# Kernel optimization log

Measured on AMD Instinct MI355X. Metric: run time of the kernel, lower is better.

The kernel has to match this reference:

```python
import jax, jax.numpy as jnp
import numpy as np

B, T, E = 2, 2048, 1024   # batch, block_size, emb_d
H, D = 16, 64             # heads, head_size


def setup_inputs() -> dict:
    key = jax.random.key(0)
    ks = jax.random.split(key, 7)
    s = 1.0 / np.sqrt(E)
    inputs = jax.random.normal(ks[0], (B, T, E), dtype=jnp.float32)
    k_w = jax.random.uniform(ks[1], (H, E, D), jnp.float32, -s, s)
    k_b = jax.random.uniform(ks[2], (H, D), jnp.float32, -s, s)
    q_w = jax.random.uniform(ks[3], (H, E, D), jnp.float32, -s, s)
    q_b = jax.random.uniform(ks[4], (H, D), jnp.float32, -s, s)
    v_w = jax.random.uniform(ks[5], (H, E, D), jnp.float32, -s, s)
    v_b = jax.random.uniform(ks[6], (H, D), jnp.float32, -s, s)
    return {"inputs": inputs, "k_w": k_w, "k_b": k_b,
            "q_w": q_w, "q_b": q_b, "v_w": v_w, "v_b": v_b}


def reference(inputs, k_w, k_b, q_w, q_b, v_w, v_b):
    # Per-head linear projections, vectorized over heads: (B,T,E)x(H,E,D)->(B,H,T,D)
    k = jnp.einsum('bte,hed->bhtd', inputs, k_w) + k_b[None, :, None, :]
    q = jnp.einsum('bte,hed->bhtd', inputs, q_w) + q_b[None, :, None, :]
    v = jnp.einsum('bte,hed->bhtd', inputs, v_w) + v_b[None, :, None, :]

    scale = D ** (-0.5)
    # scores: (B,H,Tq,Tk)
    w = jnp.einsum('bhtd,bhsd->bhts', q, k) * scale
    tril = jnp.tril(jnp.ones((T, T), dtype=bool))
    w = jnp.where(tril[None, None, :, :], w, -jnp.inf)
    # NOTE: original torch code does softmax(weights, dim=1) on a (B,T,T)
    # tensor, i.e. over the QUERY axis. Faithfully reproduce: axis=-2 here.
    w = jax.nn.softmax(w, axis=-2)
    out = jnp.einsum('bhts,bhsd->bhtd', w, v)           # (B,H,T,D)
    # concat heads along last dim, head-major order matching torch.cat
    return out.transpose(0, 2, 1, 3).reshape(B, T, H * D)
```

## Files before the change

### kernel.cpp

```cpp
#include <hip/hip_runtime.h>
#include <hip/hip_bf16.h>
#include <math.h>

#define B_ 2
#define T_ 2048
#define E_ 1024
#define H_ 16
#define D_ 64
#define NT_ 32
#define QSCALE 0.180336880f

typedef __attribute__((ext_vector_type(8))) short bf16x8;
typedef __attribute__((ext_vector_type(4))) float f32x4;

#if __has_builtin(__builtin_amdgcn_exp2f)
#define EXP2(x) __builtin_amdgcn_exp2f(x)
#else
#define EXP2(x) exp2f(x)
#endif

__device__ __forceinline__ unsigned short f2bf(float x) {
  union { float f; unsigned u; } v; v.f = x;
  unsigned r = v.u + 0x7FFFu + ((v.u >> 16) & 1u);
  return (unsigned short)(r >> 16);
}
__device__ __forceinline__ unsigned pk2bf(float a, float b) {
  __hip_bfloat162 h = __float22bfloat162_rn(make_float2(a, b));
  union { __hip_bfloat162 h; unsigned u; } c; c.h = h; return c.u;
}

__device__ __forceinline__ void dma8(const unsigned short* g, int gstride,
                                     unsigned short* l, int lane)
{
  const int r = lane >> 3, bg = (lane & 7) ^ (r & 7);
  __builtin_amdgcn_global_load_lds(
      (const __attribute__((address_space(1))) void*)(g + (size_t)r * gstride + bg * 8),
      (__attribute__((address_space(3))) void*)l, 16, 0, 0);
}
__device__ __forceinline__ bf16x8 frag(const unsigned short* tile, int row, int g) {
  return *(const bf16x8*)(tile + row * 64 + (((g ^ row) & 7) << 3));
}

__global__ __launch_bounds__(256) void inpack_kernel(const float* __restrict__ in,
                                                     unsigned short* __restrict__ o) {
  const size_t i = ((size_t)blockIdx.x * 256 + threadIdx.x) * 8;
  float4 f0 = *(const float4*)(in + i);
  float4 f1 = *(const float4*)(in + i + 4);
  unsigned u[4] = { pk2bf(f0.x, f0.y), pk2bf(f0.z, f0.w),
                    pk2bf(f1.x, f1.y), pk2bf(f1.z, f1.w) };
  *(bf16x8*)(o + i) = *(const bf16x8*)u;
}

__global__ __launch_bounds__(256) void wpack_kernel(
    const float* __restrict__ qw, const float* __restrict__ kw, const float* __restrict__ vw,
    unsigned short* __restrict__ qwt, unsigned short* __restrict__ kwt,
    unsigned short* __restrict__ vwt)
{
  __shared__ float s[64][65];
  const int tid = threadIdx.x;
  const int e0 = blockIdx.x * 64, h = blockIdx.y, z = blockIdx.z;
  const float* w = (z == 0) ? qw : (z == 1) ? kw : vw;
  unsigned short* o = (z == 0) ? qwt : (z == 1) ? kwt : vwt;
  {
    const int r = tid >> 2;
    #pragma unroll
    for (int p = 0; p < 4; ++p) {
      const int c = (tid & 3) * 4 + p * 16;
      float4 f = *(const float4*)(w + ((size_t)(h * E_ + e0 + r)) * D_ + c);
      s[r][c] = f.x; s[r][c+1] = f.y; s[r][c+2] = f.z; s[r][c+3] = f.w;
    }
  }
  __syncthreads();
  {
    const int d = tid >> 2, ec = (tid & 3) * 16;
    unsigned short tmp[16];
    #pragma unroll
    for (int j = 0; j < 16; ++j) tmp[j] = f2bf(s[ec + j][d]);
    unsigned short* dst = o + ((size_t)(h * D_ + d)) * E_ + e0 + ec;
    *(bf16x8*)(dst)     = *(const bf16x8*)&tmp[0];
    *(bf16x8*)(dst + 8) = *(const bf16x8*)&tmp[8];
  }
}

__global__ __launch_bounds__(256) void proj_kernel(
    const unsigned short* __restrict__ in16,
    const unsigned short* __restrict__ qwt, const unsigned short* __restrict__ kwt,
    const unsigned short* __restrict__ vwt,
    const float* __restrict__ qb, const float* __restrict__ kb, const float* __restrict__ vb,
    unsigned short* __restrict__ qo, unsigned short* __restrict__ ko,
    unsigned short* __restrict__ vt)
{
  __shared__ __align__(16) unsigned short in_s[2][128 * 64];
  __shared__ __align__(16) unsigned short w_s[2][3][64 * 64];
  const int tid = threadIdx.x;
  const int lane = tid & 63, wv = tid >> 6;
  const int l15 = lane & 15, quad = lane >> 4;
  const int t0 = blockIdx.x * 128, h = blockIdx.y, b = blockIdx.z;
  const int bh = b * H_ + h;
  const unsigned short* wts[3] = { qwt, kwt, vwt };

  f32x4 acc[3][2][4];
  #pragma unroll
  for (int x = 0; x < 3; ++x)
    #pragma unroll
    for (int s = 0; s < 2; ++s)
      #pragma unroll
      for (int nb = 0; nb < 4; ++nb) acc[x][s][nb] = (f32x4){0.f, 0.f, 0.f, 0.f};

#define PROJ_STAGE(e0_, bi_)                                                      \
  {                                                                               \
    const unsigned short* gin = in16 + ((size_t)(b * T_ + t0)) * E_ + (e0_);      \
    _Pragma("unroll")                                                             \
    for (int p = 0; p < 4; ++p) {                                                 \
      const int br = wv * 32 + p * 8;                                             \
      dma8(gin + (size_t)br * E_, E_, &in_s[bi_][br * 64], lane);                 \
    }                                                                             \
    _Pragma("unroll")                                                             \
    for (int j = 0; j < 6; ++j) {                                                 \
      const int idx = wv * 6 + j;                                                 \
      const int x = idx >> 3, br = (idx & 7) * 8;                                 \
      dma8(wts[x] + ((size_t)(h * D_ + br)) * E_ + (e0_), E_,                     \
           &w_s[bi_][x][br * 64], lane);                                          \
    }                                                                             \
  }

  PROJ_STAGE(0, 0);
  __syncthreads();
  for (int e = 0; e < 16; ++e) {
    const int bi = e & 1;
    if (e < 15) PROJ_STAGE((e + 1) * 64, bi ^ 1);
    const unsigned short* is = in_s[bi];
    #pragma unroll
    for (int kk = 0; kk < 2; ++kk) {
      const int g0 = kk * 4 + quad;
      bf16x8 a0 = frag(is, wv * 32 + l15, g0);
      bf16x8 a1 = frag(is, wv * 32 + 16 + l15, g0);
      #pragma unroll
      for (int x = 0; x < 3; ++x) {
        const unsigned short* ws = w_s[bi][x];
        #pragma unroll
        for (int nb = 0; nb < 4; ++nb) {
          bf16x8 bfr = frag(ws, nb * 16 + l15, g0);
          if (x < 2) {
            acc[x][0][nb] = __builtin_amdgcn_mfma_f32_16x16x32_bf16(bfr, a0, acc[x][0][nb], 0, 0, 0);
            acc[x][1][nb] = __builtin_amdgcn_mfma_f32_16x16x32_bf16(bfr, a1, acc[x][1][nb], 0, 0, 0);
          } else {
            acc[x][0][nb] = __builtin_amdgcn_mfma_f32_16x16x32_bf16(a0, bfr, acc[x][0][nb], 0, 0, 0);
            acc[x][1][nb] = __builtin_amdgcn_mfma_f32_16x16x32_bf16(a1, bfr, acc[x][1][nb], 0, 0, 0);
          }
        }
      }
    }
    __syncthreads();
  }
#undef PROJ_STAGE

  const size_t obase = (size_t)bh * T_;
  #pragma unroll
  for (int x = 0; x < 2; ++x) {
    const float scl = (x == 0) ? QSCALE : 1.0f;
    const float* bias = (x == 0) ? qb : kb;
    unsigned short* outp = (x == 0) ? qo : ko;
    #pragma unroll
    for (int nb = 0; nb < 4; ++nb) {
      float bias4[4];
      *(float4*)bias4 = *(const float4*)&bias[h * D_ + nb * 16 + quad * 4];
      #pragma unroll
      for (int s = 0; s < 2; ++s) {
        const int t = t0 + wv * 32 + s * 16 + l15;
        unsigned short pk[4];
        #pragma unroll
        for (int r = 0; r < 4; ++r) pk[r] = f2bf((acc[x][s][nb][r] + bias4[r]) * scl);
        *(ushort4*)(outp + (obase + t) * D_ + nb * 16 + quad * 4) = *(const ushort4*)pk;
      }
    }
  }
  #pragma unroll
  for (int nb = 0; nb < 4; ++nb) {
    const int d = nb * 16 + l15;
    const float bvv = vb[h * D_ + d];
    #pragma unroll
    for (int s = 0; s < 2; ++s) {
      const int t = t0 + wv * 32 + s * 16 + quad * 4;
      unsigned short pk[4];
      #pragma unroll
      for (int r = 0; r < 4; ++r) pk[r] = f2bf(acc[2][s][nb][r] + bvv);
      *(ushort4*)(vt + ((size_t)(bh * D_ + d)) * T_ + t) = *(const ushort4*)pk;
    }
  }
}

__global__ __launch_bounds__(256, 6) void stats_kernel(
    const unsigned short* __restrict__ q, const unsigned short* __restrict__ k,
    float* __restrict__ lg)
{
  __shared__ __align__(16) unsigned short q_s[2][64 * 64];
  __shared__ float red[4][64];
  const int tid = threadIdx.x;
  const int lane = tid & 63, wv = tid >> 6;
  const int l15 = lane & 15, quad = lane >> 4;
  const int h = blockIdx.x, b = blockIdx.y, sa = blockIdx.z;
  const int bh = b * H_ + h;
  const int s0 = sa * 64;
  const unsigned short* qbase = q + (size_t)bh * T_ * 64;

  bf16x8 kf[4][2];
  #pragma unroll
  for (int nb = 0; nb < 4; ++nb)
    #pragma unroll
    for (int kk = 0; kk < 2; ++kk)
      kf[nb][kk] = *(const bf16x8*)(k + ((size_t)(bh * T_ + s0 + nb * 16 + l15)) * 64
                                      + kk * 32 + quad * 8);

  #pragma unroll
  for (int pp = 0; pp < 2; ++pp) {
    const int br = wv * 16 + pp * 8;
    dma8(qbase + (size_t)(sa * 64 + br) * 64, 64, &q_s[0][br * 64], lane);
  }
  __syncthreads();

  float lsum[4] = {0.f, 0.f, 0.f, 0.f};

  for (int tt = sa, i = 0; tt < NT_; ++tt, ++i) {
    const int bi = i & 1;
    if (tt + 1 < NT_) {
      #pragma unroll
      for (int pp = 0; pp < 2; ++pp) {
        const int br = wv * 16 + pp * 8;
        dma8(qbase + (size_t)((tt + 1) * 64 + br) * 64, 64, &q_s[bi ^ 1][br * 64], lane);
      }
    }
    bf16x8 a0 = frag(q_s[bi], wv * 16 + l15, quad);
    bf16x8 a1 = frag(q_s[bi], wv * 16 + l15, 4 + quad);
    f32x4 sacc[4];
    #pragma unroll
    for (int nb = 0; nb < 4; ++nb) sacc[nb] = (f32x4){0.f, 0.f, 0.f, 0.f};
    #pragma unroll
    for (int nb = 0; nb < 4; ++nb) {
      sacc[nb] = __builtin_amdgcn_mfma_f32_16x16x32_bf16(a0, kf[nb][0], sacc[nb], 0, 0, 0);
      sacc[nb] = __builtin_amdgcn_mfma_f32_16x16x32_bf16(a1, kf[nb][1], sacc[nb], 0, 0, 0);
    }
    if (tt == sa) {
      const int tbase = tt * 64 + wv * 16 + quad * 4;
      #pragma unroll
      for (int nb = 0; nb < 4; ++nb) {
        const int s = s0 + nb * 16 + l15;
        #pragma unroll
        for (int r = 0; r < 4; ++r)
          lsum[nb] += (tbase + r >= s) ? EXP2(sacc[nb][r]) : 0.f;
      }
    } else {
      #pragma unroll
      for (int nb = 0; nb < 4; ++nb)
        #pragma unroll
        for (int r = 0; r < 4; ++r) lsum[nb] += EXP2(sacc[nb][r]);
    }
    __syncthreads();
  }
  #pragma unroll
  for (int nb = 0; nb < 4; ++nb) {
    lsum[nb] += __shfl_xor(lsum[nb], 16);
    lsum[nb] += __shfl_xor(lsum[nb], 32);
  }
  if (lane < 16) {
    #pragma unroll
    for (int nb = 0; nb < 4; ++nb) red[wv][nb * 16 + lane] = lsum[nb];
  }
  __syncthreads();
  if (tid < 64) {
    const float L = red[0][tid] + red[1][tid] + red[2][tid] + red[3][tid];
    lg[(size_t)bh * T_ + s0 + tid] = -__log2f(L);
  }
}

__global__ __launch_bounds__(256, 6) void out_kernel(
    const unsigned short* __restrict__ q, const unsigned short* __restrict__ k,
    const unsigned short* __restrict__ vt, const float* __restrict__ lg,
    float* __restrict__ out)
{
  __shared__ __align__(16) unsigned short k_s[64 * 64];
  __shared__ __align__(16) unsigned short vt_s[64 * 64];
  __shared__ __align__(16) unsigned short u_s[4][16][72];
  __shared__ float lg_sh[64];
  const int tid = threadIdx.x;
  const int lane = tid & 63, wv = tid >> 6;
  const int l15 = lane & 15, quad = lane >> 4;
  const int h = blockIdx.x, b = blockIdx.y, jt = 31 - blockIdx.z;
  const int bh = b * H_ + h;
  const int t0 = jt * 64;
  const unsigned short* kbase = k + (size_t)bh * T_ * 64;
  const unsigned short* vbase = vt + (size_t)bh * D_ * T_;
  const float* lgbase = lg + (size_t)bh * T_;

  const unsigned short* qrow = q + (size_t)(bh * T_ + t0 + wv * 16 + l15) * 64;
  bf16x8 qf0 = *(const bf16x8*)(qrow + quad * 8);
  bf16x8 qf1 = *(const bf16x8*)(qrow + 32 + quad * 8);

  f32x4 oacc[4];
  #pragma unroll
  for (int nb = 0; nb < 4; ++nb) oacc[nb] = (f32x4){0.f, 0.f, 0.f, 0.f};

  unsigned short* urow = &u_s[wv][l15][0];
  const int tcol = t0 + wv * 16 + l15;

  for (int st = 0; st <= jt; ++st) {
    const int s0 = st * 64;
    __syncthreads();
    #pragma unroll
    for (int pp = 0; pp < 2; ++pp) {
      const int br = wv * 16 + pp * 8;
      dma8(kbase + (size_t)(s0 + br) * 64, 64, &k_s[br * 64], lane);
      dma8(vbase + (size_t)br * T_ + s0, T_, &vt_s[br * 64], lane);
    }
    if (tid < 64) lg_sh[tid] = lgbase[s0 + tid];
    __syncthreads();
    f32x4 sacc[4];
    #pragma unroll
    for (int mb = 0; mb < 4; ++mb) {
      float lg4[4];
      *(float4*)lg4 = *(const float4*)&lg_sh[mb * 16 + quad * 4];
      sacc[mb] = (f32x4){lg4[0], lg4[1], lg4[2], lg4[3]};
    }
    #pragma unroll
    for (int mb = 0; mb < 4; ++mb) {
      bf16x8 ka0 = frag(k_s, mb * 16 + l15, quad);
      bf16x8 ka1 = frag(k_s, mb * 16 + l15, 4 + quad);
      sacc[mb] = __builtin_amdgcn_mfma_f32_16x16x32_bf16(ka0, qf0, sacc[mb], 0, 0, 0);
      sacc[mb] = __builtin_amdgcn_mfma_f32_16x16x32_bf16(ka1, qf1, sacc[mb], 0, 0, 0);
    }
    if (st == jt) {
      #pragma unroll
      for (int mb = 0; mb < 4; ++mb) {
        const int sbase = s0 + mb * 16 + quad * 4;
        float uu[4] = { EXP2(sacc[mb][0]), EXP2(sacc[mb][1]),
                        EXP2(sacc[mb][2]), EXP2(sacc[mb][3]) };
        #pragma unroll
        for (int r = 0; r < 4; ++r) if (tcol < sbase + r) uu[r] = 0.f;
        *(uint2*)(urow + mb * 16 + quad * 4) =
            make_uint2(pk2bf(uu[0], uu[1]), pk2bf(uu[2], uu[3]));
      }
    } else {
      #pragma unroll
      for (int mb = 0; mb < 4; ++mb) {
        float uu[4] = { EXP2(sacc[mb][0]), EXP2(sacc[mb][1]),
                        EXP2(sacc[mb][2]), EXP2(sacc[mb][3]) };
        *(uint2*)(urow + mb * 16 + quad * 4) =
            make_uint2(pk2bf(uu[0], uu[1]), pk2bf(uu[2], uu[3]));
      }
    }
    #pragma unroll
    for (int kk = 0; kk < 2; ++kk) {
      bf16x8 ua = *(const bf16x8*)(urow + kk * 32 + quad * 8);
      #pragma unroll
      for (int nb = 0; nb < 4; ++nb)
        oacc[nb] = __builtin_amdgcn_mfma_f32_16x16x32_bf16(
            frag(vt_s, nb * 16 + l15, kk * 4 + quad), ua, oacc[nb], 0, 0, 0);
    }
  }
  float* orow = out + ((size_t)(b * T_ + t0 + wv * 16 + l15)) * (H_ * D_) + h * D_;
  #pragma unroll
  for (int nb = 0; nb < 4; ++nb) {
    float o4[4] = { oacc[nb][0], oacc[nb][1], oacc[nb][2], oacc[nb][3] };
    *(float4*)(orow + nb * 16 + quad * 4) = *(const float4*)o4;
  }
}

extern "C" void kernel_launch(void* const* d_in, const int* in_sizes, int n_in,
                              void* d_out, int out_size, void* d_ws, size_t ws_size,
                              hipStream_t stream) {
  const float* in = (const float*)d_in[0];
  const float* kw = (const float*)d_in[1];
  const float* kb = (const float*)d_in[2];
  const float* qw = (const float*)d_in[3];
  const float* qb = (const float*)d_in[4];
  const float* vw = (const float*)d_in[5];
  const float* vb = (const float*)d_in[6];
  float* out = (float*)d_out;

  unsigned short* p = (unsigned short*)d_ws;
  const size_t inz = (size_t)B_ * T_ * E_;
  const size_t wz  = (size_t)H_ * D_ * E_;
  const size_t qz  = (size_t)B_ * H_ * T_ * D_;
  unsigned short* in16 = p;            p += inz;
  unsigned short* qwt  = p;            p += wz;
  unsigned short* kwt  = p;            p += wz;
  unsigned short* vwt  = p;            p += wz;
  unsigned short* q16  = p;            p += qz;
  unsigned short* k16  = p;            p += qz;
  unsigned short* vtb  = p;            p += qz;
  float* lgbuf = (float*)p;

  dim3 blk(256);
  inpack_kernel<<<dim3(inz / 2048), blk, 0, stream>>>(in, in16);
  wpack_kernel <<<dim3(E_ / 64, H_, 3), blk, 0, stream>>>(qw, kw, vw, qwt, kwt, vwt);
  proj_kernel  <<<dim3(T_ / 128, H_, B_), blk, 0, stream>>>(in16, qwt, kwt, vwt,
                                                            qb, kb, vb, q16, k16, vtb);
  stats_kernel <<<dim3(H_, B_, NT_), blk, 0, stream>>>(q16, k16, lgbuf);
  out_kernel   <<<dim3(H_, B_, NT_), blk, 0, stream>>>(q16, k16, vtb, lgbuf, out);
}
```

Measured before the change: 180.2 us.

## Merge pack kernels, re-tile projection per wave, double-buffer out_kernel K/V loads

Folds the input and weight bf16 pack kernels into one launch, saving a launch. The projection kernel is re-tiled so each wave owns 16 output features across all 128 tokens. This cuts weight-fragment LDS reads per wave but raises input-fragment reads and register use. out_kernel now double-buffers its K, V^T and log-sum tiles so the next tile's DMA overlaps the current tile's compute, at the cost of twice the LDS. The occupancy hints (256,6) are dropped from the stats and out kernels.

```diff
diff --git a/kernel.cpp b/kernel.cpp
--- a/kernel.cpp
+++ b/kernel.cpp
@@ -41,24 +41,25 @@
   return *(const bf16x8*)(tile + row * 64 + (((g ^ row) & 7) << 3));
 }
 
-__global__ __launch_bounds__(256) void inpack_kernel(const float* __restrict__ in,
-                                                     unsigned short* __restrict__ o) {
-  const size_t i = ((size_t)blockIdx.x * 256 + threadIdx.x) * 8;
-  float4 f0 = *(const float4*)(in + i);
-  float4 f1 = *(const float4*)(in + i + 4);
-  unsigned u[4] = { pk2bf(f0.x, f0.y), pk2bf(f0.z, f0.w),
-                    pk2bf(f1.x, f1.y), pk2bf(f1.z, f1.w) };
-  *(bf16x8*)(o + i) = *(const bf16x8*)u;
-}
-
-__global__ __launch_bounds__(256) void wpack_kernel(
+__global__ __launch_bounds__(256) void pack_kernel(
+    const float* __restrict__ in, unsigned short* __restrict__ o16,
     const float* __restrict__ qw, const float* __restrict__ kw, const float* __restrict__ vw,
     unsigned short* __restrict__ qwt, unsigned short* __restrict__ kwt,
     unsigned short* __restrict__ vwt)
 {
   __shared__ float s[64][65];
   const int tid = threadIdx.x;
-  const int e0 = blockIdx.x * 64, h = blockIdx.y, z = blockIdx.z;
+  if (blockIdx.x < 2048) {
+    const size_t i = ((size_t)blockIdx.x * 256 + tid) * 8;
+    float4 f0 = *(const float4*)(in + i);
+    float4 f1 = *(const float4*)(in + i + 4);
+    unsigned u[4] = { pk2bf(f0.x, f0.y), pk2bf(f0.z, f0.w),
+                      pk2bf(f1.x, f1.y), pk2bf(f1.z, f1.w) };
+    *(bf16x8*)(o16 + i) = *(const bf16x8*)u;
+    return;
+  }
+  const int i = blockIdx.x - 2048;
+  const int e0 = (i & 15) * 64, h = (i >> 4) & 15, z = i >> 8;
   const float* w = (z == 0) ? qw : (z == 1) ? kw : vw;
   unsigned short* o = (z == 0) ? qwt : (z == 1) ? kwt : vwt;
   {
@@ -91,7 +92,7 @@
     unsigned short* __restrict__ vt)
 {
   __shared__ __align__(16) unsigned short in_s[2][128 * 64];
-  __shared__ __align__(16) unsigned short w_s[2][3][64 * 64];
+  __shared__ __align__(16) unsigned short w_s[2][3 * 64 * 64];
   const int tid = threadIdx.x;
   const int lane = tid & 63, wv = tid >> 6;
   const int l15 = lane & 15, quad = lane >> 4;
@@ -99,13 +100,11 @@
   const int bh = b * H_ + h;
   const unsigned short* wts[3] = { qwt, kwt, vwt };
 
-  f32x4 acc[3][2][4];
+  f32x4 acc[3][8];
   #pragma unroll
   for (int x = 0; x < 3; ++x)
     #pragma unroll
-    for (int s = 0; s < 2; ++s)
-      #pragma unroll
-      for (int nb = 0; nb < 4; ++nb) acc[x][s][nb] = (f32x4){0.f, 0.f, 0.f, 0.f};
+    for (int tb = 0; tb < 8; ++tb) acc[x][tb] = (f32x4){0.f, 0.f, 0.f, 0.f};
 
 #define PROJ_STAGE(e0_, bi_)                                                      \
   {                                                                               \
@@ -120,7 +119,7 @@
       const int idx = wv * 6 + j;                                                 \
       const int x = idx >> 3, br = (idx & 7) * 8;                                 \
       dma8(wts[x] + ((size_t)(h * D_ + br)) * E_ + (e0_), E_,                     \
-           &w_s[bi_][x][br * 64], lane);                                          \
+           &w_s[bi_][x * 4096 + br * 64], lane);                                  \
     }                                                                             \
   }
 
@@ -130,25 +129,23 @@
     const int bi = e & 1;
     if (e < 15) PROJ_STAGE((e + 1) * 64, bi ^ 1);
     const unsigned short* is = in_s[bi];
+    const unsigned short* ws = w_s[bi];
     #pragma unroll
     for (int kk = 0; kk < 2; ++kk) {
       const int g0 = kk * 4 + quad;
-      bf16x8 a0 = frag(is, wv * 32 + l15, g0);
-      bf16x8 a1 = frag(is, wv * 32 + 16 + l15, g0);
-      #pragma unroll
-      for (int x = 0; x < 3; ++x) {
-        const unsigned short* ws = w_s[bi][x];
-        #pragma unroll
-        for (int nb = 0; nb < 4; ++nb) {
-          bf16x8 bfr = frag(ws, nb * 16 + l15, g0);
-          if (x < 2) {
-            acc[x][0][nb] = __builtin_amdgcn_mfma_f32_16x16x32_bf16(bfr, a0, acc[x][0][nb], 0, 0, 0);
-            acc[x][1][nb] = __builtin_amdgcn_mfma_f32_16x16x32_bf16(bfr, a1, acc[x][1][nb], 0, 0, 0);
-          } else {
-            acc[x][0][nb] = __builtin_amdgcn_mfma_f32_16x16x32_bf16(a0, bfr, acc[x][0][nb], 0, 0, 0);
-            acc[x][1][nb] = __builtin_amdgcn_mfma_f32_16x16x32_bf16(a1, bfr, acc[x][1][nb], 0, 0, 0);
-          }
-        }
+      bf16x8 bfr[3];
+      #pragma unroll
+      for (int x = 0; x < 3; ++x)
+        bfr[x] = frag(ws, x * 64 + wv * 16 + l15, g0);
+      bf16x8 afr[8];
+      #pragma unroll
+      for (int tb = 0; tb < 8; ++tb)
+        afr[tb] = frag(is, tb * 16 + l15, g0);
+      #pragma unroll
+      for (int tb = 0; tb < 8; ++tb) {
+        acc[0][tb] = __builtin_amdgcn_mfma_f32_16x16x32_bf16(bfr[0], afr[tb], acc[0][tb], 0, 0, 0);
+        acc[1][tb] = __builtin_amdgcn_mfma_f32_16x16x32_bf16(bfr[1], afr[tb], acc[1][tb], 0, 0, 0);
+        acc[2][tb] = __builtin_amdgcn_mfma_f32_16x16x32_bf16(afr[tb], bfr[2], acc[2][tb], 0, 0, 0);
       }
     }
     __syncthreads();
@@ -161,36 +158,32 @@
     const float scl = (x == 0) ? QSCALE : 1.0f;
     const float* bias = (x == 0) ? qb : kb;
     unsigned short* outp = (x == 0) ? qo : ko;
-    #pragma unroll
-    for (int nb = 0; nb < 4; ++nb) {
-      float bias4[4];
-      *(float4*)bias4 = *(const float4*)&bias[h * D_ + nb * 16 + quad * 4];
-      #pragma unroll
-      for (int s = 0; s < 2; ++s) {
-        const int t = t0 + wv * 32 + s * 16 + l15;
-        unsigned short pk[4];
-        #pragma unroll
-        for (int r = 0; r < 4; ++r) pk[r] = f2bf((acc[x][s][nb][r] + bias4[r]) * scl);
-        *(ushort4*)(outp + (obase + t) * D_ + nb * 16 + quad * 4) = *(const ushort4*)pk;
-      }
-    }
-  }
-  #pragma unroll
-  for (int nb = 0; nb < 4; ++nb) {
-    const int d = nb * 16 + l15;
+    float bias4[4];
+    *(float4*)bias4 = *(const float4*)&bias[h * D_ + wv * 16 + quad * 4];
+    #pragma unroll
+    for (int tb = 0; tb < 8; ++tb) {
+      const int t = t0 + tb * 16 + l15;
+      unsigned short pk[4];
+      #pragma unroll
+      for (int r = 0; r < 4; ++r) pk[r] = f2bf((acc[x][tb][r] + bias4[r]) * scl);
+      *(ushort4*)(outp + (obase + t) * D_ + wv * 16 + quad * 4) = *(const ushort4*)pk;
+    }
+  }
+  {
+    const int d = wv * 16 + l15;
     const float bvv = vb[h * D_ + d];
     #pragma unroll
-    for (int s = 0; s < 2; ++s) {
-      const int t = t0 + wv * 32 + s * 16 + quad * 4;
+    for (int tb = 0; tb < 8; ++tb) {
+      const int t = t0 + tb * 16 + quad * 4;
       unsigned short pk[4];
       #pragma unroll
-      for (int r = 0; r < 4; ++r) pk[r] = f2bf(acc[2][s][nb][r] + bvv);
+      for (int r = 0; r < 4; ++r) pk[r] = f2bf(acc[2][tb][r] + bvv);
       *(ushort4*)(vt + ((size_t)(bh * D_ + d)) * T_ + t) = *(const ushort4*)pk;
     }
   }
 }
 
-__global__ __launch_bounds__(256, 6) void stats_kernel(
+__global__ __launch_bounds__(256) void stats_kernel(
     const unsigned short* __restrict__ q, const unsigned short* __restrict__ k,
     float* __restrict__ lg)
 {
@@ -273,15 +266,15 @@
   }
 }
 
-__global__ __launch_bounds__(256, 6) void out_kernel(
+__global__ __launch_bounds__(256) void out_kernel(
     const unsigned short* __restrict__ q, const unsigned short* __restrict__ k,
     const unsigned short* __restrict__ vt, const float* __restrict__ lg,
     float* __restrict__ out)
 {
-  __shared__ __align__(16) unsigned short k_s[64 * 64];
-  __shared__ __align__(16) unsigned short vt_s[64 * 64];
+  __shared__ __align__(16) unsigned short k_s[2][64 * 64];
+  __shared__ __align__(16) unsigned short vt_s[2][64 * 64];
   __shared__ __align__(16) unsigned short u_s[4][16][72];
-  __shared__ float lg_sh[64];
+  __shared__ float lg_sh[2][64];
   const int tid = threadIdx.x;
   const int lane = tid & 63, wv = tid >> 6;
   const int l15 = lane & 15, quad = lane >> 4;
@@ -296,6 +289,15 @@
   bf16x8 qf0 = *(const bf16x8*)(qrow + quad * 8);
   bf16x8 qf1 = *(const bf16x8*)(qrow + 32 + quad * 8);
 
+  #pragma unroll
+  for (int pp = 0; pp < 2; ++pp) {
+    const int br = wv * 16 + pp * 8;
+    dma8(kbase + (size_t)br * 64, 64, &k_s[0][br * 64], lane);
+    dma8(vbase + (size_t)br * T_, T_, &vt_s[0][br * 64], lane);
+  }
+  if (tid < 64) lg_sh[0][tid] = lgbase[tid];
+  __syncthreads();
+
   f32x4 oacc[4];
   #pragma unroll
   for (int nb = 0; nb < 4; ++nb) oacc[nb] = (f32x4){0.f, 0.f, 0.f, 0.f};
@@ -304,27 +306,32 @@
   const int tcol = t0 + wv * 16 + l15;
 
   for (int st = 0; st <= jt; ++st) {
+    const int bi = st & 1;
+    if (st < jt) {
+      const int s1 = (st + 1) * 64;
+      #pragma unroll
+      for (int pp = 0; pp < 2; ++pp) {
+        const int br = wv * 16 + pp * 8;
+        dma8(kbase + (size_t)(s1 + br) * 64, 64, &k_s[bi ^ 1][br * 64], lane);
+        dma8(vbase + (size_t)br * T_ + s1, T_, &vt_s[bi ^ 1][br * 64], lane);
+      }
+      if (tid < 64) lg_sh[bi ^ 1][tid] = lgbase[s1 + tid];
+    }
     const int s0 = st * 64;
-    __syncthreads();
-    #pragma unroll
-    for (int pp = 0; pp < 2; ++pp) {
-      const int br = wv * 16 + pp * 8;
-      dma8(kbase + (size_t)(s0 + br) * 64, 64, &k_s[br * 64], lane);
-      dma8(vbase + (size_t)br * T_ + s0, T_, &vt_s[br * 64], lane);
-    }
-    if (tid < 64) lg_sh[tid] = lgbase[s0 + tid];
-    __syncthreads();
+    const unsigned short* ks = k_s[bi];
+    const unsigned short* vs = vt_s[bi];
+    const float* lgb = lg_sh[bi];
     f32x4 sacc[4];
     #pragma unroll
     for (int mb = 0; mb < 4; ++mb) {
       float lg4[4];
-      *(float4*)lg4 = *(const float4*)&lg_sh[mb * 16 + quad * 4];
+      *(float4*)lg4 = *(const float4*)&lgb[mb * 16 + quad * 4];
       sacc[mb] = (f32x4){lg4[0], lg4[1], lg4[2], lg4[3]};
     }
     #pragma unroll
     for (int mb = 0; mb < 4; ++mb) {
-      bf16x8 ka0 = frag(k_s, mb * 16 + l15, quad);
-      bf16x8 ka1 = frag(k_s, mb * 16 + l15, 4 + quad);
+      bf16x8 ka0 = frag(ks, mb * 16 + l15, quad);
+      bf16x8 ka1 = frag(ks, mb * 16 + l15, 4 + quad);
       sacc[mb] = __builtin_amdgcn_mfma_f32_16x16x32_bf16(ka0, qf0, sacc[mb], 0, 0, 0);
       sacc[mb] = __builtin_amdgcn_mfma_f32_16x16x32_bf16(ka1, qf1, sacc[mb], 0, 0, 0);
     }
@@ -354,8 +361,9 @@
       #pragma unroll
       for (int nb = 0; nb < 4; ++nb)
         oacc[nb] = __builtin_amdgcn_mfma_f32_16x16x32_bf16(
-            frag(vt_s, nb * 16 + l15, kk * 4 + quad), ua, oacc[nb], 0, 0, 0);
-    }
+            frag(vs, nb * 16 + l15, kk * 4 + quad), ua, oacc[nb], 0, 0, 0);
+    }
+    __syncthreads();
   }
   float* orow = out + ((size_t)(b * T_ + t0 + wv * 16 + l15)) * (H_ * D_) + h * D_;
   #pragma unroll
@@ -391,10 +399,9 @@
   float* lgbuf = (float*)p;
 
   dim3 blk(256);
-  inpack_kernel<<<dim3(inz / 2048), blk, 0, stream>>>(in, in16);
-  wpack_kernel <<<dim3(E_ / 64, H_, 3), blk, 0, stream>>>(qw, kw, vw, qwt, kwt, vwt);
-  proj_kernel  <<<dim3(T_ / 128, H_, B_), blk, 0, stream>>>(in16, qwt, kwt, vwt,
-                                                            qb, kb, vb, q16, k16, vtb);
-  stats_kernel <<<dim3(H_, B_, NT_), blk, 0, stream>>>(q16, k16, lgbuf);
-  out_kernel   <<<dim3(H_, B_, NT_), blk, 0, stream>>>(q16, k16, vtb, lgbuf, out);
-}
+  pack_kernel <<<dim3(2048 + 768), blk, 0, stream>>>(in, in16, qw, kw, vw, qwt, kwt, vwt);
+  proj_kernel <<<dim3(T_ / 128, H_, B_), blk, 0, stream>>>(in16, qwt, kwt, vwt,
+                                                           qb, kb, vb, q16, k16, vtb);
+  stats_kernel<<<dim3(H_, B_, NT_), blk, 0, stream>>>(q16, k16, lgbuf);
+  out_kernel  <<<dim3(H_, B_, NT_), blk, 0, stream>>>(q16, k16, vtb, lgbuf, out);
+}
```

Result: faster. 170.9 us (-5.2%).
